# Performance work log

Measured on AMD Instinct MI355X. Metric: run time of the kernel, lower is better.

The kernel has to match this reference:

```python
import math
import jax, jax.numpy as jnp
import numpy as np

B, H, L, D = 32, 8, 4096, 64
FACTOR = 5


def setup_inputs() -> dict:
    key = jax.random.key(0)
    kq, kk, kv, ki = jax.random.split(key, 4)
    U_part = min(FACTOR * int(math.ceil(math.log(L))), L)  # 45
    return {
        "queries": jax.random.normal(kq, (B, H, L, D), jnp.float32),
        "keys": jax.random.normal(kk, (B, H, L, D), jnp.float32),
        "values": jax.random.normal(kv, (B, H, L, D), jnp.float32),
        "index_sample": jax.random.randint(ki, (L, U_part), 0, L),
        "attn_mask": jnp.ones((1,), bool),  # presence flag only
    }


def reference(queries, keys, values, index_sample, attn_mask):
    Bq, Hq, L_Q, Dd = queries.shape
    L_K = keys.shape[2]
    u = min(FACTOR * int(math.ceil(math.log(L_Q))), L_Q)
    scale = 1.0 / math.sqrt(Dd)

    # --- _prob_QK: sample K columns per query, score sparsity measure M ---
    K_sample = jnp.take(keys, index_sample, axis=2)            # [B,H,L_Q,sample_k,D]
    Q_K_sample = jnp.einsum('bhqd,bhqkd->bhqk', queries, K_sample)
    M = Q_K_sample.max(axis=-1) - Q_K_sample.mean(axis=-1)     # [B,H,L_Q]
    M_top = jnp.argsort(M, axis=-1)[:, :, -u:]                 # [B,H,u]
    Q_reduce = jnp.take_along_axis(queries, M_top[..., None], axis=2)  # [B,H,u,D]
    scores = jnp.einsum('bhqd,bhkd->bhqk', Q_reduce, keys) * scale      # [B,H,u,L_K]

    # --- ProbMask (mask_flag=True, attn_mask present): causal mask gathered at M_top ---
    causal = jnp.triu(jnp.ones((L_Q, L_K), dtype=bool), k=1)   # [L_Q,L_K]
    mask = causal[M_top]                                       # [B,H,u,L_K]
    scores = jnp.where(mask, -jnp.inf, scores)

    attn = jax.nn.softmax(scores, axis=-1)                     # [B,H,u,L_K]

    # --- initial context: cumulative sum of V (causal mean surrogate) ---
    context = jnp.cumsum(values, axis=2)                       # [B,H,L_Q,D]

    # --- scatter the attended values at the selected top-u query positions ---
    bi = jnp.arange(Bq)[:, None, None]
    hi = jnp.arange(Hq)[None, :, None]
    upd = jnp.einsum('bhqk,bhkd->bhqd', attn, values)          # [B,H,u,D]
    context = context.at[bi, hi, M_top].set(upd)

    return jnp.transpose(context, (0, 2, 1, 3))                # [B,L_Q,H,D]
```

## Files before the change

### kernel.cpp

```cpp
#include <hip/hip_runtime.h>
#include <hip/hip_bf16.h>

#define B_  32
#define H_  8
#define L_  4096
#define D_  64
#define BH_ 256
#define U_  45
#define UP_ 48

typedef float f32x4  __attribute__((ext_vector_type(4)));
typedef short bf16x8 __attribute__((ext_vector_type(8)));

__device__ __forceinline__ unsigned short f2bf(float f) {
  unsigned u = __builtin_bit_cast(unsigned, f);
  u += 0x7fffu + ((u >> 16) & 1u);
  return (unsigned short)(u >> 16);
}

__global__ __launch_bounds__(256) void k_probM(
    const float* __restrict__ Qg, const float* __restrict__ Kg,
    const int* __restrict__ idxg, float* __restrict__ Mg)
{
  const int blk   = blockIdx.x;
  const int xcd   = blk & 7;
  const int rr    = blk >> 3;
  const int bhi   = rr >> 6;
  const int chunk = rr & 63;
  const int bh    = xcd + (bhi << 3);
  const int quad  = threadIdx.x >> 2;
  const int lq    = threadIdx.x & 3;
  const int q     = chunk * 64 + quad;

  const float* qrow = Qg + ((size_t)bh * L_ + q) * D_ + lq * 16;
  double qd[16];
#pragma unroll
  for (int c = 0; c < 4; c++) {
    f32x4 v = *(const f32x4*)(qrow + 4 * c);
    qd[4*c+0] = (double)v[0]; qd[4*c+1] = (double)v[1];
    qd[4*c+2] = (double)v[2]; qd[4*c+3] = (double)v[3];
  }

  const float* kb = Kg + (size_t)bh * L_ * D_ + lq * 16;
  const int*   ip = idxg + q * U_;

  double mx = -1e300, sm = 0.0;
  for (int j = 0; j < U_; j++) {
    const float* kr = kb + (size_t)ip[j] * D_;
    double acc = 0.0;
#pragma unroll
    for (int c = 0; c < 4; c++) {
      f32x4 v = *(const f32x4*)(kr + 4 * c);
      acc += qd[4*c+0] * (double)v[0];
      acc += qd[4*c+1] * (double)v[1];
      acc += qd[4*c+2] * (double)v[2];
      acc += qd[4*c+3] * (double)v[3];
    }
    acc += __shfl_xor(acc, 1);
    acc += __shfl_xor(acc, 2);
    mx = fmax(mx, acc);
    sm += acc;
  }
  if (lq == 0) Mg[(size_t)bh * L_ + q] = (float)(mx - sm / 45.0);
}

__global__ __launch_bounds__(256) void k_top45(
    const float* __restrict__ Mg, int* __restrict__ qselg)
{
  __shared__ float mv[L_];
  __shared__ float rv[256];
  __shared__ int   ri[256];
  __shared__ int   sels[UP_];
  const int bh = blockIdx.x, t = threadIdx.x;

  for (int i = t; i < L_; i += 256) mv[i] = Mg[(size_t)bh * L_ + i];
  __syncthreads();

  for (int it = 0; it < U_; it++) {
    float bv = -3.4e38f; int bi = 0;
    for (int i = t; i < L_; i += 256) {
      float v = mv[i];
      if (v > bv) { bv = v; bi = i; }
    }
    rv[t] = bv; ri[t] = bi;
    __syncthreads();
    for (int s = 128; s > 0; s >>= 1) {
      if (t < s) {
        float ov = rv[t + s];
        if (ov > rv[t] || (ov == rv[t] && ri[t + s] < ri[t])) {
          rv[t] = ov; ri[t] = ri[t + s];
        }
      }
      __syncthreads();
    }
    if (t == 0) { sels[it] = ri[0]; mv[ri[0]] = -3.4e38f; }
    __syncthreads();
  }
  if (t == 0) { sels[45] = sels[0]; sels[46] = sels[0]; sels[47] = sels[0]; }
  __syncthreads();
  if (t < UP_) qselg[bh * UP_ + t] = sels[t];
}

__global__ __launch_bounds__(512) void k_cumsum(
    const float* __restrict__ Vg, float* __restrict__ out)
{
  const int bh = blockIdx.x, b = bh >> 3, h = bh & 7;
  const int d = threadIdx.x & 63, s = threadIdx.x >> 6;
  __shared__ float segsum[8][64];

  const float* vb = Vg + (size_t)bh * L_ * D_ + d;
  const int l0 = s * 512;

  float acc = 0.f;
  for (int l = l0; l < l0 + 512; l += 4) {
    float a0 = vb[(size_t)(l + 0) * D_];
    float a1 = vb[(size_t)(l + 1) * D_];
    float a2 = vb[(size_t)(l + 2) * D_];
    float a3 = vb[(size_t)(l + 3) * D_];
    acc += a0; acc += a1; acc += a2; acc += a3;
  }
  segsum[s][d] = acc;
  __syncthreads();

  float run = 0.f;
  for (int ss = 0; ss < s; ss++) run += segsum[ss][d];

  float* ob = out + ((size_t)b * L_ * H_ + h) * D_ + d;
  for (int l = l0; l < l0 + 512; l += 4) {
    float a0 = vb[(size_t)(l + 0) * D_];
    float a1 = vb[(size_t)(l + 1) * D_];
    float a2 = vb[(size_t)(l + 2) * D_];
    float a3 = vb[(size_t)(l + 3) * D_];
    run += a0; ob[(size_t)(l + 0) * (H_ * D_)] = run;
    run += a1; ob[(size_t)(l + 1) * (H_ * D_)] = run;
    run += a2; ob[(size_t)(l + 2) * (H_ * D_)] = run;
    run += a3; ob[(size_t)(l + 3) * (H_ * D_)] = run;
  }
}

__global__ __launch_bounds__(512, 2) void k_attn(
    const float* __restrict__ Qg, const float* __restrict__ Kg,
    const float* __restrict__ Vg, const int* __restrict__ qselg,
    float* __restrict__ out)
{
  const int bh = blockIdx.x, b = bh >> 3, h = bh & 7;
  const int wave = threadIdx.x >> 6, lane = threadIdx.x & 63;
  const int l15 = lane & 15, l4 = lane >> 4;

  __shared__ int   qs[UP_];
  __shared__ float mw[8][UP_];
  __shared__ float lw[8][UP_];
  __shared__ float lgf[UP_];
  __shared__ float Osum[UP_][64];
  __shared__ unsigned short Pl[8][16][72];

  if (threadIdx.x < UP_) qs[threadIdx.x] = qselg[bh * UP_ + threadIdx.x];
  for (int i = threadIdx.x; i < UP_ * 64; i += 512) (&Osum[0][0])[i] = 0.f;
  __syncthreads();

  int qmax = 0;
  for (int r2 = 0; r2 < UP_; r2++) qmax = max(qmax, qs[r2]);

  const float* Qb = Qg + (size_t)bh * L_ * D_;
  const float* Kb = Kg + (size_t)bh * L_ * D_;
  const float* Vb = Vg + (size_t)bh * L_ * D_;

  bf16x8 aq[3][2];
#pragma unroll
  for (int mf = 0; mf < 3; mf++) {
    const float* src = Qb + (size_t)qs[mf * 16 + l15] * D_ + l4 * 8;
#pragma unroll
    for (int ks = 0; ks < 2; ks++) {
      bf16x8 a;
#pragma unroll
      for (int j = 0; j < 8; j++) a[j] = (short)f2bf(src[ks * 32 + j]);
      aq[mf][ks] = a;
    }
  }

  int myq[3][4];
#pragma unroll
  for (int mf = 0; mf < 3; mf++)
#pragma unroll
    for (int rg = 0; rg < 4; rg++)
      myq[mf][rg] = qs[mf * 16 + l4 * 4 + rg];

  float m_r[3][4], l_r[3][4];
  f32x4 Oa[3][4];
  const f32x4 z4 = {0.f, 0.f, 0.f, 0.f};
#pragma unroll
  for (int mf = 0; mf < 3; mf++)
#pragma unroll
    for (int rg = 0; rg < 4; rg++) { m_r[mf][rg] = -1e30f; l_r[mf][rg] = 0.f; }
#pragma unroll
  for (int mf = 0; mf < 3; mf++)
#pragma unroll
    for (int df = 0; df < 4; df++) Oa[mf][df] = z4;

  for (int t = 0; t < 8; t++) {
    const int k0 = wave * 512 + t * 64;
    if (k0 > qmax) break;

    f32x4 S[3][4];
#pragma unroll
    for (int nf = 0; nf < 4; nf++) {
      const float* ksrc = Kb + (size_t)(k0 + nf * 16 + l15) * D_ + l4 * 8;
      bf16x8 bk0, bk1;
#pragma unroll
      for (int j = 0; j < 8; j++) bk0[j] = (short)f2bf(ksrc[j]);
#pragma unroll
      for (int j = 0; j < 8; j++) bk1[j] = (short)f2bf(ksrc[32 + j]);
#pragma unroll
      for (int mf = 0; mf < 3; mf++) {
        f32x4 c = z4;
        c = __builtin_amdgcn_mfma_f32_16x16x32_bf16(aq[mf][0], bk0, c, 0, 0, 0);
        c = __builtin_amdgcn_mfma_f32_16x16x32_bf16(aq[mf][1], bk1, c, 0, 0, 0);
        S[mf][nf] = c;
      }
    }

#pragma unroll
    for (int mf = 0; mf < 3; mf++)
#pragma unroll
      for (int nf = 0; nf < 4; nf++) {
        const int kc = k0 + nf * 16 + l15;
#pragma unroll
        for (int rg = 0; rg < 4; rg++) {
          float v = S[mf][nf][rg] * 0.125f;
          S[mf][nf][rg] = (kc > myq[mf][rg]) ? -1e30f : v;
        }
      }

    bf16x8 vv[2][4];
#pragma unroll
    for (int ks = 0; ks < 2; ks++)
#pragma unroll
      for (int df = 0; df < 4; df++) {
        bf16x8 x;
#pragma unroll
        for (int j = 0; j < 8; j++)
          x[j] = (short)f2bf(Vb[(size_t)(k0 + ks * 32 + l4 * 8 + j) * D_ + df * 16 + l15]);
        vv[ks][df] = x;
      }

#pragma unroll
    for (int mf = 0; mf < 3; mf++) {
#pragma unroll
      for (int rg = 0; rg < 4; rg++) {
        float tm = fmax(fmax(S[mf][0][rg], S[mf][1][rg]),
                        fmax(S[mf][2][rg], S[mf][3][rg]));
#pragma unroll
        for (int off = 1; off < 16; off <<= 1) tm = fmax(tm, __shfl_xor(tm, off));
        const float mn = fmax(m_r[mf][rg], tm);
        const float sc = __expf(m_r[mf][rg] - mn);
        l_r[mf][rg] *= sc;
#pragma unroll
        for (int df = 0; df < 4; df++) Oa[mf][df][rg] *= sc;
        m_r[mf][rg] = mn;
      }

      float rs[4] = {0.f, 0.f, 0.f, 0.f};
#pragma unroll
      for (int nf = 0; nf < 4; nf++)
#pragma unroll
        for (int rg = 0; rg < 4; rg++) {
          float p = __expf(S[mf][nf][rg] - m_r[mf][rg]);
          p = (m_r[mf][rg] > -1e29f) ? p : 0.f;
          rs[rg] += p;
          Pl[wave][l4 * 4 + rg][nf * 16 + l15] = f2bf(p);
        }
#pragma unroll
      for (int rg = 0; rg < 4; rg++) {
        float r = rs[rg];
#pragma unroll
        for (int off = 1; off < 16; off <<= 1) r += __shfl_xor(r, off);
        l_r[mf][rg] += r;
      }

#pragma unroll
      for (int ks = 0; ks < 2; ks++) {
        const bf16x8 pa = *(const bf16x8*)(&Pl[wave][l15][ks * 32 + l4 * 8]);
#pragma unroll
        for (int df = 0; df < 4; df++)
          Oa[mf][df] = __builtin_amdgcn_mfma_f32_16x16x32_bf16(pa, vv[ks][df], Oa[mf][df], 0, 0, 0);
      }
    }
  }

  if (l15 == 0) {
#pragma unroll
    for (int mf = 0; mf < 3; mf++)
#pragma unroll
      for (int rg = 0; rg < 4; rg++) {
        const int row = mf * 16 + l4 * 4 + rg;
        mw[wave][row] = m_r[mf][rg];
        lw[wave][row] = l_r[mf][rg];
      }
  }
  __syncthreads();

  float sc_me[3][4];
#pragma unroll
  for (int mf = 0; mf < 3; mf++)
#pragma unroll
    for (int rg = 0; rg < 4; rg++) {
      const int row = mf * 16 + l4 * 4 + rg;
      float m = -1e30f;
#pragma unroll
      for (int w = 0; w < 8; w++) m = fmax(m, mw[w][row]);
      float ls = 0.f;
#pragma unroll
      for (int w = 0; w < 8; w++) ls += lw[w][row] * __expf(mw[w][row] - m);
      sc_me[mf][rg] = __expf(m_r[mf][rg] - m);
      if (wave == 0 && l15 == 0) lgf[row] = ls;
    }

  for (int w = 0; w < 8; w++) {
    __syncthreads();
    if (wave == w) {
#pragma unroll
      for (int mf = 0; mf < 3; mf++)
#pragma unroll
        for (int df = 0; df < 4; df++)
#pragma unroll
          for (int rg = 0; rg < 4; rg++)
            Osum[mf * 16 + l4 * 4 + rg][df * 16 + l15] += Oa[mf][df][rg] * sc_me[mf][rg];
    }
  }
  __syncthreads();

  for (int i = threadIdx.x; i < U_ * 64; i += 512) {
    const int r = i >> 6, d = i & 63;
    out[(((size_t)b * L_ + (size_t)qs[r]) * H_ + h) * D_ + d] = Osum[r][d] / lgf[r];
  }
}

extern "C" void kernel_launch(void* const* d_in, const int* in_sizes, int n_in,
                              void* d_out, int out_size, void* d_ws, size_t ws_size,
                              hipStream_t stream)
{
  const float* Q   = (const float*)d_in[0];
  const float* K   = (const float*)d_in[1];
  const float* V   = (const float*)d_in[2];
  const int*   idx = (const int*)d_in[3];
  float* out = (float*)d_out;

  const size_t m_bytes = (size_t)BH_ * L_ * sizeof(float);
  float* M    = (float*)d_ws;
  int*   qsel = (int*)((char*)d_ws + m_bytes);
  if (ws_size < m_bytes + (size_t)BH_ * UP_ * sizeof(int)) return;

  k_probM <<<16384, 256, 0, stream>>>(Q, K, idx, M);
  k_top45 <<<BH_,   256, 0, stream>>>(M, qsel);
  k_cumsum<<<BH_,   512, 0, stream>>>(V, out);
  k_attn  <<<BH_,   512, 0, stream>>>(Q, K, V, qsel, out);
}
```

Baseline: 1.286 ms.

## Rewrite sampled QK scoring in fp32 with one lane per sampled key

The sparsity-measure kernel drops fp64 accumulation for fp32 FMAs and remaps work so each wave lane handles one of the 45 sampled keys for a query, with max and sum done by a 64-wide shuffle reduction. Query rows are staged in shared memory, and each block covers 32 queries with 8 per wave, so the grid doubles. This removes slow double-precision arithmetic and the serial 45-iteration loop. In exchange, a quarter of the lanes sit idle, each lane loads a full 256-byte key row, and the lower precision may change the top-u selection when M values are nearly tied.

```diff
diff --git a/kernel.cpp b/kernel.cpp
--- a/kernel.cpp
+++ b/kernel.cpp
@@ -25,43 +25,63 @@
   const int blk   = blockIdx.x;
   const int xcd   = blk & 7;
   const int rr    = blk >> 3;
-  const int bhi   = rr >> 6;
-  const int chunk = rr & 63;
+  const int bhi   = rr >> 7;
+  const int chunk = rr & 127;
   const int bh    = xcd + (bhi << 3);
-  const int quad  = threadIdx.x >> 2;
-  const int lq    = threadIdx.x & 3;
-  const int q     = chunk * 64 + quad;
-
-  const float* qrow = Qg + ((size_t)bh * L_ + q) * D_ + lq * 16;
-  double qd[16];
-#pragma unroll
-  for (int c = 0; c < 4; c++) {
-    f32x4 v = *(const f32x4*)(qrow + 4 * c);
-    qd[4*c+0] = (double)v[0]; qd[4*c+1] = (double)v[1];
-    qd[4*c+2] = (double)v[2]; qd[4*c+3] = (double)v[3];
-  }
-
-  const float* kb = Kg + (size_t)bh * L_ * D_ + lq * 16;
-  const int*   ip = idxg + q * U_;
-
-  double mx = -1e300, sm = 0.0;
-  for (int j = 0; j < U_; j++) {
-    const float* kr = kb + (size_t)ip[j] * D_;
-    double acc = 0.0;
+  const int q0    = chunk * 32;
+
+  const int wave = threadIdx.x >> 6;
+  const int lane = threadIdx.x & 63;
+  const int j    = (lane < U_) ? lane : (U_ - 1);
+
+  __shared__ float qbuf[32][64];
+  {
+    const f32x4* src = (const f32x4*)(Qg + ((size_t)bh * L_ + q0) * D_);
+    f32x4* dst = (f32x4*)qbuf;
+    for (int i = threadIdx.x; i < 32 * 64 / 4; i += 256) dst[i] = src[i];
+  }
+  __syncthreads();
+
+  const float* Kb = Kg + (size_t)bh * (L_ * D_);
+
+  for (int qi = 0; qi < 8; qi++) {
+    const int qq = wave * 8 + qi;
+    const int q  = q0 + qq;
+
+    const int kid = idxg[(size_t)q * U_ + j];
+    const float* kr = Kb + (size_t)kid * D_;
+
+    float dacc = 0.f;
 #pragma unroll
     for (int c = 0; c < 4; c++) {
-      f32x4 v = *(const f32x4*)(kr + 4 * c);
-      acc += qd[4*c+0] * (double)v[0];
-      acc += qd[4*c+1] * (double)v[1];
-      acc += qd[4*c+2] * (double)v[2];
-      acc += qd[4*c+3] * (double)v[3];
-    }
-    acc += __shfl_xor(acc, 1);
-    acc += __shfl_xor(acc, 2);
-    mx = fmax(mx, acc);
-    sm += acc;
-  }
-  if (lq == 0) Mg[(size_t)bh * L_ + q] = (float)(mx - sm / 45.0);
+      f32x4 k0 = *(const f32x4*)(kr + c * 16);
+      f32x4 k1 = *(const f32x4*)(kr + c * 16 + 4);
+      f32x4 k2 = *(const f32x4*)(kr + c * 16 + 8);
+      f32x4 k3 = *(const f32x4*)(kr + c * 16 + 12);
+      const float* qp = &qbuf[qq][c * 16];
+      f32x4 p0 = *(const f32x4*)(qp);
+      f32x4 p1 = *(const f32x4*)(qp + 4);
+      f32x4 p2 = *(const f32x4*)(qp + 8);
+      f32x4 p3 = *(const f32x4*)(qp + 12);
+      dacc = fmaf(k0[0], p0[0], dacc); dacc = fmaf(k0[1], p0[1], dacc);
+      dacc = fmaf(k0[2], p0[2], dacc); dacc = fmaf(k0[3], p0[3], dacc);
+      dacc = fmaf(k1[0], p1[0], dacc); dacc = fmaf(k1[1], p1[1], dacc);
+      dacc = fmaf(k1[2], p1[2], dacc); dacc = fmaf(k1[3], p1[3], dacc);
+      dacc = fmaf(k2[0], p2[0], dacc); dacc = fmaf(k2[1], p2[1], dacc);
+      dacc = fmaf(k2[2], p2[2], dacc); dacc = fmaf(k2[3], p2[3], dacc);
+      dacc = fmaf(k3[0], p3[0], dacc); dacc = fmaf(k3[1], p3[1], dacc);
+      dacc = fmaf(k3[2], p3[2], dacc); dacc = fmaf(k3[3], p3[3], dacc);
+    }
+
+    float mxv = (lane < U_) ? dacc : -3.4e38f;
+    float smv = (lane < U_) ? dacc : 0.f;
+#pragma unroll
+    for (int off = 1; off < 64; off <<= 1) {
+      mxv = fmax(mxv, __shfl_xor(mxv, off));
+      smv += __shfl_xor(smv, off);
+    }
+    if (lane == 0) Mg[(size_t)bh * L_ + q] = mxv - smv * (1.0f / 45.0f);
+  }
 }
 
 __global__ __launch_bounds__(256) void k_top45(
@@ -350,7 +370,7 @@
   int*   qsel = (int*)((char*)d_ws + m_bytes);
   if (ws_size < m_bytes + (size_t)BH_ * UP_ * sizeof(int)) return;
 
-  k_probM <<<16384, 256, 0, stream>>>(Q, K, idx, M);
+  k_probM <<<32768, 256, 0, stream>>>(Q, K, idx, M);
   k_top45 <<<BH_,   256, 0, stream>>>(M, qsel);
   k_cumsum<<<BH_,   512, 0, stream>>>(V, out);
   k_attn  <<<BH_,   512, 0, stream>>>(Q, K, V, qsel, out);
```

Measured after the change: 1.962 ms. 52.6% more time.

## Bucket sampled indices by key chunk and stream K through LDS for probM

Applied to the files above, without the earlier changes.

Adds a single-block prep kernel that sorts the (query, sampled key) pairs into cells keyed by key chunk and query range. The probM kernel then streams K in 256-row chunks into double-buffered LDS via global_load_lds and scores each bucketed pair against the LDS copy. This replaces the scattered per-query global gathers of K rows. Dot products move from double to float, and max and sum are accumulated as fixed-point integer LDS atomics, which adds quantisation and could change the top-u selection on near ties. The one-block prep kernel is a serial cost and recomputes the same bucketing on every call.

```diff
diff --git a/kernel.cpp b/kernel.cpp
--- a/kernel.cpp
+++ b/kernel.cpp
@@ -9,7 +9,15 @@
 #define U_  45
 #define UP_ 48
 
+#define CHUNK_R 256
+#define NCH     16
+#define QCH     1024
+#define NQC     4
+#define NCELLS  1024
+#define NENT    (L_ * U_)
+
 typedef float f32x4  __attribute__((ext_vector_type(4)));
+typedef float f32x2  __attribute__((ext_vector_type(2)));
 typedef short bf16x8 __attribute__((ext_vector_type(8)));
 
 __device__ __forceinline__ unsigned short f2bf(float f) {
@@ -18,50 +26,140 @@
   return (unsigned short)(u >> 16);
 }
 
-__global__ __launch_bounds__(256) void k_probM(
+__global__ __launch_bounds__(1024) void k_prep(
+    const int* __restrict__ idxg, unsigned* __restrict__ cellbase,
+    unsigned* __restrict__ entries)
+{
+  __shared__ unsigned cnt[NCELLS];
+  const int t = threadIdx.x;
+  cnt[t] = 0u;
+  __syncthreads();
+  for (int i = t; i < NENT; i += 1024) {
+    const int q = i / U_;
+    const int v = idxg[i];
+    const int cell = ((v >> 8) << 6) | (q >> 6);
+    atomicAdd(&cnt[cell], 1u);
+  }
+  __syncthreads();
+  if (t == 0) {
+    unsigned run = 0;
+    for (int c = 0; c < NCELLS; c++) { cellbase[c] = run; run += cnt[c]; }
+    cellbase[NCELLS] = run;
+  }
+  __syncthreads();
+  cnt[t] = cellbase[t];
+  __syncthreads();
+  for (int i = t; i < NENT; i += 1024) {
+    const int q = i / U_;
+    const int v = idxg[i];
+    const int cell = ((v >> 8) << 6) | (q >> 6);
+    const unsigned slot = atomicAdd(&cnt[cell], 1u);
+    entries[slot] = ((unsigned)q << 8) | (unsigned)(v & 255);
+  }
+}
+
+__global__ __launch_bounds__(1024) void k_probM(
     const float* __restrict__ Qg, const float* __restrict__ Kg,
-    const int* __restrict__ idxg, float* __restrict__ Mg)
-{
-  const int blk   = blockIdx.x;
-  const int xcd   = blk & 7;
-  const int rr    = blk >> 3;
-  const int bhi   = rr >> 6;
-  const int chunk = rr & 63;
-  const int bh    = xcd + (bhi << 3);
-  const int quad  = threadIdx.x >> 2;
-  const int lq    = threadIdx.x & 3;
-  const int q     = chunk * 64 + quad;
-
-  const float* qrow = Qg + ((size_t)bh * L_ + q) * D_ + lq * 16;
-  double qd[16];
-#pragma unroll
-  for (int c = 0; c < 4; c++) {
-    f32x4 v = *(const f32x4*)(qrow + 4 * c);
-    qd[4*c+0] = (double)v[0]; qd[4*c+1] = (double)v[1];
-    qd[4*c+2] = (double)v[2]; qd[4*c+3] = (double)v[3];
-  }
-
-  const float* kb = Kg + (size_t)bh * L_ * D_ + lq * 16;
-  const int*   ip = idxg + q * U_;
-
-  double mx = -1e300, sm = 0.0;
-  for (int j = 0; j < U_; j++) {
-    const float* kr = kb + (size_t)ip[j] * D_;
-    double acc = 0.0;
-#pragma unroll
-    for (int c = 0; c < 4; c++) {
-      f32x4 v = *(const f32x4*)(kr + 4 * c);
-      acc += qd[4*c+0] * (double)v[0];
-      acc += qd[4*c+1] * (double)v[1];
-      acc += qd[4*c+2] * (double)v[2];
-      acc += qd[4*c+3] * (double)v[3];
-    }
-    acc += __shfl_xor(acc, 1);
-    acc += __shfl_xor(acc, 2);
-    mx = fmax(mx, acc);
-    sm += acc;
-  }
-  if (lq == 0) Mg[(size_t)bh * L_ + q] = (float)(mx - sm / 45.0);
+    const unsigned* __restrict__ cellbase, const unsigned* __restrict__ entries,
+    float* __restrict__ Mg)
+{
+  const int bid = blockIdx.x;
+  const int xcd = bid & 7, kk = bid >> 3;
+  const int bh  = xcd + ((kk >> 2) << 3);
+  const int qc  = kk & 3;
+
+  __shared__ float kbuf[2][CHUNK_R * 64];
+  __shared__ int                smax[QCH];
+  __shared__ unsigned long long ssum[QCH];
+
+  const int t = threadIdx.x;
+  smax[t] = (int)0x80000000;
+  ssum[t] = 0ull;
+
+  const float* Kb = Kg + (size_t)bh * (L_ * D_);
+
+#define STAGE(KC, BSEL) do { \
+    _Pragma("unroll") \
+    for (int uu = 0; uu < 4; uu++) { \
+      const int l_  = t + uu * 1024; \
+      const int r_  = l_ >> 4, p_ = l_ & 15; \
+      const int us_ = p_ ^ (r_ & 15); \
+      const float* src_ = Kb + ((size_t)((KC) * CHUNK_R + r_)) * 64 + us_ * 4; \
+      __builtin_amdgcn_global_load_lds( \
+          (const __attribute__((address_space(1))) void*)src_, \
+          (__attribute__((address_space(3))) void*)(&kbuf[BSEL][0] + l_ * 4), \
+          16, 0, 0); \
+    } \
+  } while (0)
+
+  STAGE(0, 0);
+  __syncthreads();
+
+  const int quad = t >> 2, lq = t & 3;
+  const int qf0  = qc * 16;
+
+  for (int kc = 0; kc < NCH; kc++) {
+    const int cur = kc & 1;
+    if (kc + 1 < NCH) STAGE(kc + 1, cur ^ 1);
+
+    const unsigned e0 = cellbase[(kc << 6) + qf0];
+    const unsigned e1 = cellbase[(kc << 6) + qf0 + 16];
+
+    for (unsigned e = e0 + quad; e < e1; e += 256) {
+      const unsigned ent = entries[e];
+      const int q = (int)(ent >> 8);
+      const int r = (int)(ent & 255u);
+
+      const float* qp = Qg + ((size_t)bh * L_ + q) * 64 + lq * 16;
+      const f32x4 qa = *(const f32x4*)(qp);
+      const f32x4 qb = *(const f32x4*)(qp + 4);
+      const f32x4 qcv= *(const f32x4*)(qp + 8);
+      const f32x4 qd = *(const f32x4*)(qp + 12);
+
+      const float* kb0 = &kbuf[cur][r * 64];
+      const int rx = r & 15;
+      const int u0 = (lq * 4 + 0) ^ rx;
+      const int u1 = (lq * 4 + 1) ^ rx;
+      const int u2 = (lq * 4 + 2) ^ rx;
+      const int u3 = (lq * 4 + 3) ^ rx;
+      const f32x2 k0a = *(const f32x2*)(kb0 + u0 * 4);
+      const f32x2 k0b = *(const f32x2*)(kb0 + u0 * 4 + 2);
+      const f32x2 k1a = *(const f32x2*)(kb0 + u1 * 4);
+      const f32x2 k1b = *(const f32x2*)(kb0 + u1 * 4 + 2);
+      const f32x2 k2a = *(const f32x2*)(kb0 + u2 * 4);
+      const f32x2 k2b = *(const f32x2*)(kb0 + u2 * 4 + 2);
+      const f32x2 k3a = *(const f32x2*)(kb0 + u3 * 4);
+      const f32x2 k3b = *(const f32x2*)(kb0 + u3 * 4 + 2);
+
+      float d0 = 0.f, d1 = 0.f;
+      d0 = fmaf(qa[0], k0a[0], d0); d1 = fmaf(qa[1], k0a[1], d1);
+      d0 = fmaf(qa[2], k0b[0], d0); d1 = fmaf(qa[3], k0b[1], d1);
+      d0 = fmaf(qb[0], k1a[0], d0); d1 = fmaf(qb[1], k1a[1], d1);
+      d0 = fmaf(qb[2], k1b[0], d0); d1 = fmaf(qb[3], k1b[1], d1);
+      d0 = fmaf(qcv[0], k2a[0], d0); d1 = fmaf(qcv[1], k2a[1], d1);
+      d0 = fmaf(qcv[2], k2b[0], d0); d1 = fmaf(qcv[3], k2b[1], d1);
+      d0 = fmaf(qd[0], k3a[0], d0); d1 = fmaf(qd[1], k3a[1], d1);
+      d0 = fmaf(qd[2], k3b[0], d0); d1 = fmaf(qd[3], k3b[1], d1);
+      float dot = d0 + d1;
+      dot += __shfl_xor(dot, 1);
+      dot += __shfl_xor(dot, 2);
+
+      if (lq == 0) {
+        const int fx = (int)rintf(dot * 1048576.0f);
+        atomicMax(&smax[q & (QCH - 1)], fx);
+        atomicAdd(&ssum[q & (QCH - 1)], (unsigned long long)(long long)fx);
+      }
+    }
+    __syncthreads();
+  }
+#undef STAGE
+
+  {
+    const double inv = 1.0 / 1048576.0;
+    const double mx = (double)smax[t] * inv;
+    const double sm = (double)(long long)ssum[t] * inv;
+    Mg[(size_t)bh * L_ + qc * QCH + t] = (float)(mx - sm / 45.0);
+  }
 }
 
 __global__ __launch_bounds__(256) void k_top45(
@@ -345,13 +443,21 @@
   const int*   idx = (const int*)d_in[3];
   float* out = (float*)d_out;
 
-  const size_t m_bytes = (size_t)BH_ * L_ * sizeof(float);
-  float* M    = (float*)d_ws;
-  int*   qsel = (int*)((char*)d_ws + m_bytes);
-  if (ws_size < m_bytes + (size_t)BH_ * UP_ * sizeof(int)) return;
-
-  k_probM <<<16384, 256, 0, stream>>>(Q, K, idx, M);
-  k_top45 <<<BH_,   256, 0, stream>>>(M, qsel);
-  k_cumsum<<<BH_,   512, 0, stream>>>(V, out);
-  k_attn  <<<BH_,   512, 0, stream>>>(Q, K, V, qsel, out);
-}
+  const size_t m_bytes    = (size_t)BH_ * L_ * sizeof(float);
+  const size_t qsel_bytes = (size_t)BH_ * UP_ * sizeof(int);
+  const size_t ent_bytes  = (size_t)NENT * sizeof(unsigned);
+  const size_t cb_bytes   = (size_t)(NCELLS + 1) * sizeof(unsigned);
+
+  char* p = (char*)d_ws;
+  float*    M        = (float*)p;                 p += m_bytes;
+  int*      qsel     = (int*)p;                   p += qsel_bytes;
+  unsigned* entries  = (unsigned*)p;              p += ent_bytes;
+  unsigned* cellbase = (unsigned*)p;              p += cb_bytes;
+  if (ws_size < (size_t)(p - (char*)d_ws)) return;
+
+  k_prep  <<<1,    1024, 0, stream>>>(idx, cellbase, entries);
+  k_probM <<<1024, 1024, 0, stream>>>(Q, K, cellbase, entries, M);
+  k_top45 <<<BH_,  256,  0, stream>>>(M, qsel);
+  k_cumsum<<<BH_,  512,  0, stream>>>(V, out);
+  k_attn  <<<BH_,  512,  0, stream>>>(Q, K, V, qsel, out);
+}
```

New measurement: 1.472 ms. 1.15x slower.
